# Kernel optimization log

Measured on AMD Instinct MI355X. Metric: run time of the kernel, lower is better.

## Reference

```python
import jax, jax.numpy as jnp
import numpy as np

N_EMBD = 512
N_HEADS = 8
D_HEAD = N_EMBD // N_HEADS


def setup_inputs() -> dict:
    key = jax.random.key(0)
    k1, k2, k3, k4, k5 = jax.random.split(key, 5)
    B, T = 4, 2048
    scale = 1.0 / np.sqrt(N_EMBD)
    return {
        "x": jax.random.normal(k1, (B, T, N_EMBD), dtype=jnp.float32),
        # fused QKV projection: Linear(n_embd, 3*n_embd)
        "W_attn": jax.random.normal(k2, (N_EMBD, 3 * N_EMBD), dtype=jnp.float32) * scale,
        "b_attn": jax.random.normal(k3, (3 * N_EMBD,), dtype=jnp.float32) * 0.01,
        # output projection: Linear(n_embd, n_embd)
        "W_out": jax.random.normal(k4, (N_EMBD, N_EMBD), dtype=jnp.float32) * scale,
        "b_out": jax.random.normal(k5, (N_EMBD,), dtype=jnp.float32) * 0.01,
    }


def reference(x, W_attn, b_attn, W_out, b_out):
    B, T, C = x.shape
    # fused QKV projection then split
    qkv = x @ W_attn + b_attn  # [B, T, 3C]
    q, k, v = jnp.split(qkv, 3, axis=-1)
    # [B, T, C] -> [B, H, T, Dh]
    def heads(t):
        return t.reshape(B, T, N_HEADS, D_HEAD).transpose(0, 2, 1, 3)
    q, k, v = heads(q), heads(k), heads(v)
    # scaled dot-product attention (non-causal, no mask; dropout off in eval)
    scores = jnp.einsum("bhqd,bhkd->bhqk", q, k) / jnp.sqrt(jnp.float32(D_HEAD))
    attn = jax.nn.softmax(scores, axis=-1)
    y = jnp.einsum("bhqk,bhkd->bhqd", attn, v)  # [B, H, T, Dh]
    y = y.transpose(0, 2, 1, 3).reshape(B, T, C)
    # output projection (resid dropout off in eval)
    return y @ W_out + b_out
```

## Files before the change

### kernel.cpp

```cpp
#include <hip/hip_runtime.h>

typedef __attribute__((ext_vector_type(8))) short bf16x8;
typedef __attribute__((ext_vector_type(4))) float f32x4;
typedef unsigned short u16;
typedef unsigned int u32;

#define MFMA16(A, B, C) __builtin_amdgcn_mfma_f32_16x16x32_bf16((A), (B), (C), 0, 0, 0)

#if __has_builtin(__builtin_amdgcn_exp2f)
#define EXP2(x) __builtin_amdgcn_exp2f(x)
#else
#define EXP2(x) exp2f(x)
#endif

typedef __attribute__((address_space(3))) unsigned int lds_u32;
typedef const __attribute__((address_space(1))) unsigned int glb_u32;

__device__ __forceinline__ u16 f2bf(float f) {
  union { float f; unsigned u; } x; x.f = f;
  unsigned r = (x.u + 0x7fffu + ((x.u >> 16) & 1u)) >> 16;
  return (u16)r;
}
__device__ __forceinline__ float bf2f(u16 h) {
  union { float f; unsigned u; } x; x.u = ((unsigned)h) << 16;
  return x.f;
}

__device__ __forceinline__ void stage_sw64(const u16* src, u16* lds, int tid) {
#pragma unroll
  for (int i = 0; i < 2; i++) {
    int vv = tid + i * 256;
    int row = vv >> 3, c = vv & 7;
    const u16* gp = src + (size_t)row * 64 + (size_t)(c ^ (row & 7)) * 8;
    __builtin_amdgcn_global_load_lds((glb_u32*)gp,
        (lds_u32*)(lds + (size_t)(i * 256 + (tid & 192)) * 8), 16, 0, 0);
  }
}


__global__ __launch_bounds__(256) void cast_x_kernel(const float* __restrict__ x,
                                                     u16* __restrict__ xb, int n4) {
  int i = blockIdx.x * 256 + threadIdx.x;
  if (i >= n4) return;
  float4 v = ((const float4*)x)[i];
  ushort4 o;
  o.x = f2bf(v.x); o.y = f2bf(v.y); o.z = f2bf(v.z); o.w = f2bf(v.w);
  ((ushort4*)xb)[i] = o;
}

__global__ __launch_bounds__(256) void trans_wa_kernel(const float* __restrict__ W,
                                                       u16* __restrict__ wta) {
  __shared__ u16 T[64][72];
  const int n0 = blockIdx.x * 64;
  const int k0 = blockIdx.y * 64;
  const int tid = threadIdx.x;
  const int r = tid >> 4, c4 = (tid & 15) * 4;
#pragma unroll
  for (int i = 0; i < 4; i++) {
    int row = r + i * 16;
    float4 v = *(const float4*)&W[(size_t)(k0 + row) * 1536 + n0 + c4];
    T[c4 + 0][row] = f2bf(v.x);
    T[c4 + 1][row] = f2bf(v.y);
    T[c4 + 2][row] = f2bf(v.z);
    T[c4 + 3][row] = f2bf(v.w);
  }
  __syncthreads();
  const int row = tid >> 2, c16 = (tid & 3) * 16;
  *(uint4*)&wta[(size_t)(n0 + row) * 512 + k0 + c16]     = *(uint4*)&T[row][c16];
  *(uint4*)&wta[(size_t)(n0 + row) * 512 + k0 + c16 + 8] = *(uint4*)&T[row][c16 + 8];
}

__global__ __launch_bounds__(256) void trans_wo_kernel(const float* __restrict__ W,
                                                       u16* __restrict__ whi,
                                                       u16* __restrict__ wlo) {
  __shared__ u16 Th[64][72];
  __shared__ u16 Tl[64][72];
  const int n0 = blockIdx.x * 64;
  const int k0 = blockIdx.y * 64;
  const int tid = threadIdx.x;
  const int r = tid >> 4, c4 = (tid & 15) * 4;
#pragma unroll
  for (int i = 0; i < 4; i++) {
    int row = r + i * 16;
    float4 v = *(const float4*)&W[(size_t)(k0 + row) * 512 + n0 + c4];
    float vv[4] = {v.x, v.y, v.z, v.w};
#pragma unroll
    for (int jj = 0; jj < 4; jj++) {
      u16 hi = f2bf(vv[jj]);
      Th[c4 + jj][row] = hi;
      Tl[c4 + jj][row] = f2bf(vv[jj] - bf2f(hi));
    }
  }
  __syncthreads();
  const int row = tid >> 2, c16 = (tid & 3) * 16;
  *(uint4*)&whi[(size_t)(n0 + row) * 512 + k0 + c16]     = *(uint4*)&Th[row][c16];
  *(uint4*)&whi[(size_t)(n0 + row) * 512 + k0 + c16 + 8] = *(uint4*)&Th[row][c16 + 8];
  *(uint4*)&wlo[(size_t)(n0 + row) * 512 + k0 + c16]     = *(uint4*)&Tl[row][c16];
  *(uint4*)&wlo[(size_t)(n0 + row) * 512 + k0 + c16 + 8] = *(uint4*)&Tl[row][c16 + 8];
}

__global__ __launch_bounds__(256) void gemm_qkv(const u16* __restrict__ xb,
                                                const u16* __restrict__ wta,
                                                const float* __restrict__ b_attn,
                                                u16* __restrict__ q,
                                                u16* __restrict__ kk,
                                                u16* __restrict__ v) {
  __shared__ u16 A_lds[2][64 * 72];
  __shared__ u16 B_lds[2][64 * 72];
  const int bid = blockIdx.x;
  const int xcd = bid & 7, rr = bid >> 3;
  const int m0 = (xcd * 16 + (rr & 15)) * 64;
  const int n0 = (rr >> 4) * 64;
  const int tid  = threadIdx.x;
  const int lane = tid & 63, w = tid >> 6;
  const int wm = w >> 1, wn = w & 1;
  const int quad = lane >> 4, l15 = lane & 15;

  f32x4 acc[2][2] = {};

  uint4 ra[2], rb[2];
#pragma unroll
  for (int i = 0; i < 2; i++) {
    int vv = tid + i * 256;
    int row = vv >> 3, cv = (vv & 7) * 8;
    ra[i] = *(const uint4*)(xb  + (size_t)(m0 + row) * 512 + cv);
    rb[i] = *(const uint4*)(wta + (size_t)(n0 + row) * 512 + cv);
  }

  for (int kt = 0; kt < 8; kt++) {
    u16* Ab = A_lds[kt & 1];
    u16* Bb = B_lds[kt & 1];
#pragma unroll
    for (int i = 0; i < 2; i++) {
      int vv = tid + i * 256;
      int row = vv >> 3, cv = (vv & 7) * 8;
      *(uint4*)&Ab[row * 72 + cv] = ra[i];
      *(uint4*)&Bb[row * 72 + cv] = rb[i];
    }
    __syncthreads();
    if (kt < 7) {
      int k0 = (kt + 1) * 64;
#pragma unroll
      for (int i = 0; i < 2; i++) {
        int vv = tid + i * 256;
        int row = vv >> 3, cv = (vv & 7) * 8;
        ra[i] = *(const uint4*)(xb  + (size_t)(m0 + row) * 512 + k0 + cv);
        rb[i] = *(const uint4*)(wta + (size_t)(n0 + row) * 512 + k0 + cv);
      }
    }
#pragma unroll
    for (int ks = 0; ks < 2; ks++) {
      bf16x8 af[2], bf[2];
#pragma unroll
      for (int ri = 0; ri < 2; ri++)
        af[ri] = *(const bf16x8*)&Ab[(wm * 32 + ri * 16 + l15) * 72 + ks * 32 + quad * 8];
#pragma unroll
      for (int ci = 0; ci < 2; ci++)
        bf[ci] = *(const bf16x8*)&Bb[(wn * 32 + ci * 16 + l15) * 72 + ks * 32 + quad * 8];
#pragma unroll
      for (int ri = 0; ri < 2; ri++)
#pragma unroll
        for (int ci = 0; ci < 2; ci++)
          acc[ri][ci] = MFMA16(af[ri], bf[ci], acc[ri][ci]);
    }
  }

  const float QS = 0.18033688011112043f;
#pragma unroll
  for (int ri = 0; ri < 2; ri++) {
#pragma unroll
    for (int ci = 0; ci < 2; ci++) {
      int n = n0 + wn * 32 + ci * 16 + l15;
      float bias = b_attn[n];
      int chunk = n >> 9;
      int c = n & 511;
      int h = c >> 6, d = c & 63;
      int m_base = m0 + wm * 32 + ri * 16 + quad * 4;
      int b = m_base >> 11, t0 = m_base & 2047;
      int bh = b * 8 + h;
      if (chunk == 0) {
#pragma unroll
        for (int r = 0; r < 4; r++)
          q[(size_t)(bh * 2048 + t0 + r) * 64 + d] = f2bf((acc[ri][ci][r] + bias) * QS);
      } else if (chunk == 1) {
#pragma unroll
        for (int r = 0; r < 4; r++)
          kk[(size_t)(bh * 2048 + t0 + r) * 64 + d] = f2bf(acc[ri][ci][r] + bias);
      } else {
        int it = t0 >> 7, ks2 = (t0 >> 5) & 3, qd = (t0 >> 3) & 3, jj = t0 & 7;
        ushort4 pk;
        pk.x = f2bf(acc[ri][ci][0] + bias);
        pk.y = f2bf(acc[ri][ci][1] + bias);
        pk.z = f2bf(acc[ri][ci][2] + bias);
        pk.w = f2bf(acc[ri][ci][3] + bias);
        size_t idx = ((((size_t)bh * 16 + it) * 4 + ks2) * 64 + d) * 32 + qd * 8 + jj;
        *(ushort4*)&v[idx] = pk;
      }
    }
  }
}

__global__ __launch_bounds__(256, 4) void flash_attn(const u16* __restrict__ q,
                                                     const u16* __restrict__ k,
                                                     const u16* __restrict__ vt,
                                                     u16* __restrict__ yb) {
  __shared__ u16 K_lds[2][64 * 64];
  __shared__ u16 P_lds[4 * 16 * 136];

  const int flat = blockIdx.y * 16 + blockIdx.x;
  const int bh = (flat & 7) * 4 + ((flat >> 3) & 3);
  const int qt = flat >> 5;

  const int tid  = threadIdx.x;
  const int lane = tid & 63, w = tid >> 6;
  const int quad = lane >> 4, l15 = lane & 15;
  const int sw0 = ((quad)     ^ (l15 & 7)) * 8;
  const int sw1 = ((quad + 4) ^ (l15 & 7)) * 8;

  const u16* qp = q  + (size_t)bh * 131072;
  const u16* kp = k  + (size_t)bh * 131072;
  const u16* vp = vt + (size_t)bh * 131072;

  bf16x8 qf[2];
#pragma unroll
  for (int ks = 0; ks < 2; ks++)
    qf[ks] = *(const bf16x8*)(qp + (size_t)(qt * 64 + w * 16 + l15) * 64 + ks * 32 + quad * 8);

  f32x4 l_acc = {};
  f32x4 o[4] = {};

  bf16x8 ones;
  {
    short one = (short)0x3F80;
    ones = (bf16x8){one, one, one, one, one, one, one, one};
  }

  u16* Pw = &P_lds[w * 16 * 136];

  stage_sw64(kp, K_lds[0], tid);

  for (int it = 0; it < 32; it++) {
    __syncthreads();
    if (it < 31) stage_sw64(kp + (size_t)(it + 1) * 4096, K_lds[(it + 1) & 1], tid);
    const u16* Kb = K_lds[it & 1];
    const u16* vit = vp + it * 4096;

#pragma unroll
    for (int jt = 0; jt < 4; jt++) {
      bf16x8 kf0 = *(const bf16x8*)&Kb[(jt * 16 + l15) * 64 + sw0];
      bf16x8 kf1 = *(const bf16x8*)&Kb[(jt * 16 + l15) * 64 + sw1];
      f32x4 s = {0.f, 0.f, 0.f, 0.f};
      s = MFMA16(kf0, qf[0], s);
      s = MFMA16(kf1, qf[1], s);
      u32 pb[4];
#pragma unroll
      for (int r = 0; r < 4; r++) pb[r] = __float_as_uint(EXP2(s[r]));
      uint2 pk;
      pk.x = __builtin_amdgcn_perm(pb[1], pb[0], 0x07060302u);
      pk.y = __builtin_amdgcn_perm(pb[3], pb[2], 0x07060302u);
      *(uint2*)&Pw[l15 * 136 + jt * 16 + quad * 4] = pk;
    }

    bf16x8 vf[2][4];
#pragma unroll
    for (int dt = 0; dt < 4; dt++)
      vf[0][dt] = *(const bf16x8*)(vit + (dt * 16 + l15) * 32 + quad * 8);
#pragma unroll
    for (int ks = 0; ks < 2; ks++) {
      if (ks < 1) {
#pragma unroll
        for (int dt = 0; dt < 4; dt++)
          vf[1][dt] = *(const bf16x8*)(vit + 2048 + (dt * 16 + l15) * 32 + quad * 8);
      }
      bf16x8 pf = *(const bf16x8*)&Pw[l15 * 136 + ks * 32 + quad * 8];
      l_acc = MFMA16(pf, ones, l_acc);
#pragma unroll
      for (int dt = 0; dt < 4; dt++)
        o[dt] = MFMA16(pf, vf[ks][dt], o[dt]);
    }
  }

  const int b = bh >> 3, h = bh & 7;
  u32* Tw = (u32*)Pw;
#pragma unroll
  for (int r = 0; r < 4; r++) {
    float inv = 1.f / l_acc[r];
#pragma unroll
    for (int dt = 0; dt < 4; dt++) {
      float val = o[dt][r] * inv;
      u16 hi = f2bf(val);
      u16 lo = f2bf(val - bf2f(hi));
      Tw[(quad * 4 + r) * 68 + dt * 16 + l15] = (u32)hi | ((u32)lo << 16);
    }
  }
  {
    int t = qt * 64 + w * 16 + l15;
    size_t rowb = (size_t)(b * 2048 + t) * 512 + h * 64 + quad * 16;
    uint4 g0 = *(uint4*)&Tw[l15 * 68 + quad * 16 + 0];
    uint4 g1 = *(uint4*)&Tw[l15 * 68 + quad * 16 + 4];
    uint4 g2 = *(uint4*)&Tw[l15 * 68 + quad * 16 + 8];
    uint4 g3 = *(uint4*)&Tw[l15 * 68 + quad * 16 + 12];
    uint4 hi4, lo4;
    hi4.x = __builtin_amdgcn_perm(g0.y, g0.x, 0x05040100u);
    hi4.y = __builtin_amdgcn_perm(g0.w, g0.z, 0x05040100u);
    hi4.z = __builtin_amdgcn_perm(g1.y, g1.x, 0x05040100u);
    hi4.w = __builtin_amdgcn_perm(g1.w, g1.z, 0x05040100u);
    lo4.x = __builtin_amdgcn_perm(g0.y, g0.x, 0x07060302u);
    lo4.y = __builtin_amdgcn_perm(g0.w, g0.z, 0x07060302u);
    lo4.z = __builtin_amdgcn_perm(g1.y, g1.x, 0x07060302u);
    lo4.w = __builtin_amdgcn_perm(g1.w, g1.z, 0x07060302u);
    *(uint4*)&yb[rowb] = hi4;
    *(uint4*)&yb[(size_t)4 * 2048 * 512 + rowb] = lo4;
    hi4.x = __builtin_amdgcn_perm(g2.y, g2.x, 0x05040100u);
    hi4.y = __builtin_amdgcn_perm(g2.w, g2.z, 0x05040100u);
    hi4.z = __builtin_amdgcn_perm(g3.y, g3.x, 0x05040100u);
    hi4.w = __builtin_amdgcn_perm(g3.w, g3.z, 0x05040100u);
    lo4.x = __builtin_amdgcn_perm(g2.y, g2.x, 0x07060302u);
    lo4.y = __builtin_amdgcn_perm(g2.w, g2.z, 0x07060302u);
    lo4.z = __builtin_amdgcn_perm(g3.y, g3.x, 0x07060302u);
    lo4.w = __builtin_amdgcn_perm(g3.w, g3.z, 0x07060302u);
    *(uint4*)&yb[rowb + 8] = hi4;
    *(uint4*)&yb[(size_t)4 * 2048 * 512 + rowb + 8] = lo4;
  }
}

__global__ __launch_bounds__(256) void gemm_out(const u16* __restrict__ yhi,
                                                const u16* __restrict__ ylo,
                                                const u16* __restrict__ whi,
                                                const u16* __restrict__ wlo,
                                                const float* __restrict__ b_out,
                                                float* __restrict__ out) {
  __shared__ u16 Ah[64 * 72];
  __shared__ u16 Al[64 * 72];
  __shared__ u16 Bh[64 * 72];
  __shared__ u16 Bl[64 * 72];
  const int bid = blockIdx.x;
  const int xcd = bid & 7, rr = bid >> 3;
  const int m0 = (xcd * 16 + (rr & 15)) * 64;
  const int n0 = (rr >> 4) * 64;
  const int tid  = threadIdx.x;
  const int lane = tid & 63, w = tid >> 6;
  const int wm = w >> 1, wn = w & 1;
  const int quad = lane >> 4, l15 = lane & 15;

  f32x4 acc[2][2] = {};

  for (int k0 = 0; k0 < 512; k0 += 64) {
#pragma unroll
    for (int i = 0; i < 2; i++) {
      int vv = tid + i * 256;
      int row = vv >> 3;
      int cv  = (vv & 7) * 8;
      *(uint4*)&Ah[row * 72 + cv] = *(const uint4*)(yhi + (size_t)(m0 + row) * 512 + k0 + cv);
      *(uint4*)&Al[row * 72 + cv] = *(const uint4*)(ylo + (size_t)(m0 + row) * 512 + k0 + cv);
      *(uint4*)&Bh[row * 72 + cv] = *(const uint4*)(whi + (size_t)(n0 + row) * 512 + k0 + cv);
      *(uint4*)&Bl[row * 72 + cv] = *(const uint4*)(wlo + (size_t)(n0 + row) * 512 + k0 + cv);
    }
    __syncthreads();
#pragma unroll
    for (int ks = 0; ks < 2; ks++) {
      bf16x8 afh[2], afl[2], bfh[2], bfl[2];
#pragma unroll
      for (int ri = 0; ri < 2; ri++) {
        afh[ri] = *(const bf16x8*)&Ah[(wm * 32 + ri * 16 + l15) * 72 + ks * 32 + quad * 8];
        afl[ri] = *(const bf16x8*)&Al[(wm * 32 + ri * 16 + l15) * 72 + ks * 32 + quad * 8];
      }
#pragma unroll
      for (int ci = 0; ci < 2; ci++) {
        bfh[ci] = *(const bf16x8*)&Bh[(wn * 32 + ci * 16 + l15) * 72 + ks * 32 + quad * 8];
        bfl[ci] = *(const bf16x8*)&Bl[(wn * 32 + ci * 16 + l15) * 72 + ks * 32 + quad * 8];
      }
#pragma unroll
      for (int ri = 0; ri < 2; ri++)
#pragma unroll
        for (int ci = 0; ci < 2; ci++) {
          acc[ri][ci] = MFMA16(afh[ri], bfh[ci], acc[ri][ci]);
          acc[ri][ci] = MFMA16(afh[ri], bfl[ci], acc[ri][ci]);
          acc[ri][ci] = MFMA16(afl[ri], bfh[ci], acc[ri][ci]);
        }
    }
    __syncthreads();
  }

#pragma unroll
  for (int ri = 0; ri < 2; ri++) {
#pragma unroll
    for (int ci = 0; ci < 2; ci++) {
      int n = n0 + wn * 32 + ci * 16 + l15;
      float bias = b_out[n];
#pragma unroll
      for (int r = 0; r < 4; r++) {
        int m = m0 + wm * 32 + ri * 16 + quad * 4 + r;
        out[(size_t)m * 512 + n] = acc[ri][ci][r] + bias;
      }
    }
  }
}

extern "C" void kernel_launch(void* const* d_in, const int* in_sizes, int n_in,
                              void* d_out, int out_size, void* d_ws, size_t ws_size,
                              hipStream_t stream) {
  const float* x      = (const float*)d_in[0];
  const float* W_attn = (const float*)d_in[1];
  const float* b_attn = (const float*)d_in[2];
  const float* W_out  = (const float*)d_in[3];
  const float* b_out  = (const float*)d_in[4];
  float* out = (float*)d_out;

  char* ws = (char*)d_ws;
  u16* xb   = (u16*)(ws + 0);
  u16* wta  = (u16*)(ws + 8388608);
  u16* wtoh = (u16*)(ws + 9961472);
  u16* wtol = (u16*)(ws + 10485760);
  u16* qb   = (u16*)(ws + 11010048);
  u16* kb   = (u16*)(ws + 19398656);
  u16* vtb  = (u16*)(ws + 27787264);
  u16* yhi  = (u16*)(ws + 36175872);

  cast_x_kernel<<<4096, 256, 0, stream>>>(x, xb, 4 * 2048 * 512 / 4);
  trans_wa_kernel<<<dim3(24, 8), 256, 0, stream>>>(W_attn, wta);
  trans_wo_kernel<<<dim3(8, 8), 256, 0, stream>>>(W_out, wtoh, wtol);
  gemm_qkv<<<3072, 256, 0, stream>>>(xb, wta, b_attn, qb, kb, vtb);
  flash_attn<<<dim3(16, 64), 256, 0, stream>>>(qb, kb, vtb, yhi);
  gemm_out<<<1024, 256, 0, stream>>>(yhi, yhi + (size_t)4 * 2048 * 512, wtoh, wtol, b_out, out);
}
```

Baseline: 197.8 us.

## Software-pipeline attention loop: compute next tile's scores while doing current P·V

Restructures the flash-attention main loop into a software pipeline. Each iteration computes QK^T and exp for tile it+1 while running the P·V MFMAs for tile it. The P scratch in LDS becomes double-buffered with a narrower row stride, and K staging is issued two tiles ahead, with a prologue and epilogue added. It also raises wave priority around the P·V MFMA block so matrix work interleaves better with the exp and LDS work. Holding two tiles in flight adds register pressure under the existing launch bounds.

```diff
diff --git a/kernel.cpp b/kernel.cpp
--- a/kernel.cpp
+++ b/kernel.cpp
@@ -205,7 +205,7 @@
                                                      const u16* __restrict__ vt,
                                                      u16* __restrict__ yb) {
   __shared__ u16 K_lds[2][64 * 64];
-  __shared__ u16 P_lds[4 * 16 * 136];
+  __shared__ u16 P_lds[4 * 2 * 16 * 72];
 
   const int flat = blockIdx.y * 16 + blockIdx.x;
   const int bh = (flat & 7) * 4 + ((flat >> 3) & 3);
@@ -235,50 +235,65 @@
     ones = (bf16x8){one, one, one, one, one, one, one, one};
   }
 
-  u16* Pw = &P_lds[w * 16 * 136];
+  u16* Pw = &P_lds[w * 2 * 16 * 72];
+
+#define S_PHASE(KB, PB)                                                        \
+  do {                                                                         \
+    _Pragma("unroll")                                                          \
+    for (int jt = 0; jt < 4; jt++) {                                           \
+      bf16x8 kf0 = *(const bf16x8*)&(KB)[(jt * 16 + l15) * 64 + sw0];          \
+      bf16x8 kf1 = *(const bf16x8*)&(KB)[(jt * 16 + l15) * 64 + sw1];          \
+      f32x4 s = {0.f, 0.f, 0.f, 0.f};                                          \
+      s = MFMA16(kf0, qf[0], s);                                               \
+      s = MFMA16(kf1, qf[1], s);                                               \
+      u32 pb[4];                                                               \
+      _Pragma("unroll")                                                        \
+      for (int r = 0; r < 4; r++) pb[r] = __float_as_uint(EXP2(s[r]));         \
+      uint2 pk;                                                                \
+      pk.x = __builtin_amdgcn_perm(pb[1], pb[0], 0x07060302u);                 \
+      pk.y = __builtin_amdgcn_perm(pb[3], pb[2], 0x07060302u);                 \
+      *(uint2*)&(PB)[l15 * 72 + jt * 16 + quad * 4] = pk;                      \
+    }                                                                          \
+  } while (0)
+
+#define PV_PHASE(VIT, PB)                                                      \
+  do {                                                                         \
+    bf16x8 vf[2][4];                                                           \
+    _Pragma("unroll")                                                          \
+    for (int dt = 0; dt < 4; dt++)                                             \
+      vf[0][dt] = *(const bf16x8*)((VIT) + (dt * 16 + l15) * 32 + quad * 8);   \
+    _Pragma("unroll")                                                          \
+    for (int dt = 0; dt < 4; dt++)                                             \
+      vf[1][dt] = *(const bf16x8*)((VIT) + 2048 + (dt * 16 + l15) * 32 + quad * 8); \
+    __builtin_amdgcn_s_setprio(1);                                             \
+    _Pragma("unroll")                                                          \
+    for (int ks = 0; ks < 2; ks++) {                                           \
+      bf16x8 pf = *(const bf16x8*)&(PB)[l15 * 72 + ks * 32 + quad * 8];        \
+      l_acc = MFMA16(pf, ones, l_acc);                                         \
+      _Pragma("unroll")                                                        \
+      for (int dt = 0; dt < 4; dt++)                                           \
+        o[dt] = MFMA16(pf, vf[ks][dt], o[dt]);                                 \
+    }                                                                          \
+    __builtin_amdgcn_s_setprio(0);                                             \
+  } while (0)
 
   stage_sw64(kp, K_lds[0], tid);
-
-  for (int it = 0; it < 32; it++) {
+  stage_sw64(kp + 4096, K_lds[1], tid);
+  __syncthreads();
+  S_PHASE(K_lds[0], Pw);
+
+  for (int it = 0; it < 31; it++) {
     __syncthreads();
-    if (it < 31) stage_sw64(kp + (size_t)(it + 1) * 4096, K_lds[(it + 1) & 1], tid);
-    const u16* Kb = K_lds[it & 1];
-    const u16* vit = vp + it * 4096;
-
-#pragma unroll
-    for (int jt = 0; jt < 4; jt++) {
-      bf16x8 kf0 = *(const bf16x8*)&Kb[(jt * 16 + l15) * 64 + sw0];
-      bf16x8 kf1 = *(const bf16x8*)&Kb[(jt * 16 + l15) * 64 + sw1];
-      f32x4 s = {0.f, 0.f, 0.f, 0.f};
-      s = MFMA16(kf0, qf[0], s);
-      s = MFMA16(kf1, qf[1], s);
-      u32 pb[4];
-#pragma unroll
-      for (int r = 0; r < 4; r++) pb[r] = __float_as_uint(EXP2(s[r]));
-      uint2 pk;
-      pk.x = __builtin_amdgcn_perm(pb[1], pb[0], 0x07060302u);
-      pk.y = __builtin_amdgcn_perm(pb[3], pb[2], 0x07060302u);
-      *(uint2*)&Pw[l15 * 136 + jt * 16 + quad * 4] = pk;
-    }
-
-    bf16x8 vf[2][4];
-#pragma unroll
-    for (int dt = 0; dt < 4; dt++)
-      vf[0][dt] = *(const bf16x8*)(vit + (dt * 16 + l15) * 32 + quad * 8);
-#pragma unroll
-    for (int ks = 0; ks < 2; ks++) {
-      if (ks < 1) {
-#pragma unroll
-        for (int dt = 0; dt < 4; dt++)
-          vf[1][dt] = *(const bf16x8*)(vit + 2048 + (dt * 16 + l15) * 32 + quad * 8);
-      }
-      bf16x8 pf = *(const bf16x8*)&Pw[l15 * 136 + ks * 32 + quad * 8];
-      l_acc = MFMA16(pf, ones, l_acc);
-#pragma unroll
-      for (int dt = 0; dt < 4; dt++)
-        o[dt] = MFMA16(pf, vf[ks][dt], o[dt]);
-    }
-  }
+    if (it < 30) stage_sw64(kp + (size_t)(it + 2) * 4096, K_lds[it & 1], tid);
+    u16* Pc = Pw + (it & 1) * 16 * 72;
+    u16* Pn = Pw + ((it + 1) & 1) * 16 * 72;
+    S_PHASE(K_lds[(it + 1) & 1], Pn);
+    PV_PHASE(vp + (it) * 4096, Pc);
+  }
+  PV_PHASE(vp + 31 * 4096, Pw + (31 & 1) * 16 * 72);
+
+#undef S_PHASE
+#undef PV_PHASE
 
   const int b = bh >> 3, h = bh & 7;
   u32* Tw = (u32*)Pw;
```

Measured after the change: 196.3 us. Within noise of the previous version (-0.8%).
